# Optimization experiments

Hardware: AMD Instinct MI355X
Metric: run time of the kernel (lower is better)

## Reference

```python
import jax, jax.numpy as jnp
import numpy as np

N_HEAD = 16
N_KV_HEADS = 4
N_REP = 4
HEAD_DIM = 128
N_EMBD = 2048
EPS = 1e-5
ROPE_BASE = 10000.0


def setup_inputs() -> dict:
    key = jax.random.key(0)
    ks = jax.random.split(key, 5)
    B, T, C = 2, 2048, N_EMBD
    s = 0.02
    return {
        "x": jax.random.normal(ks[0], (B, T, C), dtype=jnp.float32),
        "wq": jax.random.normal(ks[1], (C, N_HEAD * HEAD_DIM), dtype=jnp.float32) * s,
        "wk": jax.random.normal(ks[2], (C, N_KV_HEADS * HEAD_DIM), dtype=jnp.float32) * s,
        "wv": jax.random.normal(ks[3], (C, N_KV_HEADS * HEAD_DIM), dtype=jnp.float32) * s,
        "wc": jax.random.normal(ks[4], (C, C), dtype=jnp.float32) * s,
        "q_norm_w": jnp.ones((HEAD_DIM,), dtype=jnp.float32),
        "k_norm_w": jnp.ones((HEAD_DIM,), dtype=jnp.float32),
    }


def _rmsnorm(x, w):
    # norm in fp32, scale by weight (matches RMSNorm.forward)
    xf = x.astype(jnp.float32)
    rms = jax.lax.rsqrt(jnp.mean(xf * xf, axis=-1, keepdims=True) + EPS)
    return (xf * rms).astype(x.dtype) * w


def _rope(x, cos, sin):
    # x: [B,T,H,D]; cos/sin: [T, D//2]; interleaved even/odd rotation
    xf = x.astype(jnp.float32)
    xe = xf[..., 0::2]
    xo = xf[..., 1::2]
    c = cos[None, :, None, :]
    s = sin[None, :, None, :]
    ye = xe * c - xo * s
    yo = xe * s + xo * c
    y = jnp.stack((ye, yo), axis=-1).reshape(x.shape)
    return y.astype(x.dtype)


def reference(x, wq, wk, wv, wc, q_norm_w, k_norm_w):
    B, T, C = x.shape
    q = (x @ wq).reshape(B, T, N_HEAD, HEAD_DIM)
    k = (x @ wk).reshape(B, T, N_KV_HEADS, HEAD_DIM)
    v = (x @ wv).reshape(B, T, N_KV_HEADS, HEAD_DIM)

    q = _rmsnorm(q, q_norm_w)
    k = _rmsnorm(k, k_norm_w)

    inv_freq = 1.0 / (ROPE_BASE ** (jnp.arange(0, HEAD_DIM, 2, dtype=jnp.float32) / HEAD_DIM))
    theta = jnp.arange(T, dtype=jnp.float32)[:, None] * inv_freq[None, :]  # [T, D//2]
    cos, sin = jnp.cos(theta), jnp.sin(theta)
    q = _rope(q, cos, sin)
    k = _rope(k, cos, sin)

    # GQA: repeat kv heads (repeat_kv with n_rep)
    k = jnp.repeat(k, N_REP, axis=2)  # [B,T,H,D]
    v = jnp.repeat(v, N_REP, axis=2)

    scale = 1.0 / jnp.sqrt(jnp.float32(HEAD_DIM))
    scores = jnp.einsum("bthd,bshd->bhts", q, k) * scale  # [B,H,T,S]
    causal = jnp.tril(jnp.ones((T, T), dtype=bool))
    scores = jnp.where(causal[None, None], scores, jnp.finfo(scores.dtype).min)
    attn = jax.nn.softmax(scores, axis=-1)
    y = jnp.einsum("bhts,bshd->bthd", attn, v).reshape(B, T, C)
    return y @ wc
```

## Files before the change

kernel.cpp:

```cpp
#include <hip/hip_runtime.h>
#include <hip/hip_bf16.h>
#include <cstdint>
#include <cstddef>

using bf16 = __hip_bfloat16;
typedef __attribute__((ext_vector_type(8))) short short8;
typedef __attribute__((ext_vector_type(4))) float f32x4;
typedef __attribute__((ext_vector_type(16))) float f32x16;

#define T_SEQ 2048
#define NHEAD 16
#define NKV 4
#define HD 128
#define CE 2048

__device__ __forceinline__ void gl_lds16(const void* g, void* l) {
  __builtin_amdgcn_global_load_lds(
      (const __attribute__((address_space(1))) unsigned int*)g,
      (__attribute__((address_space(3))) unsigned int*)l, 16, 0, 0);
}

__device__ __forceinline__ unsigned int cvtpk_bf16(float lo, float hi) {
  unsigned int r;
  asm("v_cvt_pk_bf16_f32 %0, %1, %2" : "=v"(r) : "v"(lo), "v"(hi));
  return r;
}

__device__ __forceinline__ void plswap(unsigned int& x, unsigned int& y, int hi) {
#if __has_builtin(__builtin_amdgcn_permlane32_swap)
  auto r = __builtin_amdgcn_permlane32_swap(x, y, false, false);
  x = r[0];
  y = r[1];
#else
  unsigned int xp = (unsigned int)__shfl_xor((int)x, 32);
  unsigned int yp = (unsigned int)__shfl_xor((int)y, 32);
  unsigned int nx = hi ? yp : x;
  unsigned int ny = hi ? y : xp;
  x = nx;
  y = ny;
#endif
}

__global__ void __launch_bounds__(256) cvt_bf16(const float* __restrict__ in,
                                                bf16* __restrict__ out, int n4) {
  const int i = blockIdx.x * blockDim.x + threadIdx.x;
  if (i >= n4) return;
  const float4 v = ((const float4*)in)[i];
  bf16 b0 = __float2bfloat16(v.x), b1 = __float2bfloat16(v.y),
       b2 = __float2bfloat16(v.z), b3 = __float2bfloat16(v.w);
  ushort4 u;
  u.x = *(const unsigned short*)&b0; u.y = *(const unsigned short*)&b1;
  u.z = *(const unsigned short*)&b2; u.w = *(const unsigned short*)&b3;
  ((ushort4*)out)[i] = u;
}

__global__ void __launch_bounds__(256) transpose_cvt(const float* __restrict__ W,
                                                     bf16* __restrict__ Wt, int N) {
  __shared__ float tile[32][33];
  const int tx = threadIdx.x & 31, ty = threadIdx.x >> 5;
  const int bx = blockIdx.x, by = blockIdx.y;
#pragma unroll
  for (int i = 0; i < 4; i++) {
    const int r = by * 32 + ty + i * 8;
    tile[ty + i * 8][tx] = W[(size_t)r * N + bx * 32 + tx];
  }
  __syncthreads();
#pragma unroll
  for (int i = 0; i < 4; i++) {
    const int n = bx * 32 + ty + i * 8;
    Wt[(size_t)n * 2048 + by * 32 + tx] = __float2bfloat16(tile[tx][ty + i * 8]);
  }
}

template <int BM, int BN, int WM, int WN>
__global__ void __launch_bounds__(512, 2)
gemm2p(const bf16* __restrict__ A, const bf16* __restrict__ Bt,
       float* __restrict__ C, int M, int N, int K) {
  constexpr int MF = BM / WM / 16;
  constexpr int NF = BN / WN / 16;
  constexpr int MH = MF / 2, NH = NF / 2;
  constexpr int AL = BM / 64;
  constexpr int BL = BN / 64;
  __shared__ bf16 smA[2][BM * 64];
  __shared__ bf16 smB[2][BN * 64];

  const int tid = threadIdx.x, lane = tid & 63, wid = tid >> 6;
  const int l15 = lane & 15, l4 = lane >> 4;
  const int wr = wid / WN, wc = wid % WN;

  const int nwg = gridDim.x;
  const int q = nwg >> 3, r = nwg & 7;
  const int xcd = blockIdx.x & 7, lin = blockIdx.x >> 3;
  const int wg = (xcd < r ? xcd * (q + 1) : r * (q + 1) + (xcd - r) * q) + lin;
  const int gw = N / BN;
  const int by = wg / gw, bx = wg % gw;
  const int row0 = by * BM, col0 = bx * BN;
  const int NT = K >> 6;

  const bf16* Ag = A + (size_t)row0 * K;
  const bf16* Bg = Bt + (size_t)col0 * K;

  auto stageA = [&](int t, int pbuf) {
    const int k0 = t << 6;
#pragma unroll
    for (int j = 0; j < AL; j++) {
      const int c = j * 512 + tid;
      const int rowi = c >> 3;
      gl_lds16(Ag + (size_t)rowi * K + k0 + (((c & 7) ^ (rowi & 7)) << 3),
               (void*)(&smA[pbuf][c << 3]));
    }
  };
  auto stageB = [&](int t, int pbuf) {
    const int k0 = t << 6;
#pragma unroll
    for (int j = 0; j < BL; j++) {
      const int c = j * 512 + tid;
      const int rowi = c >> 3;
      gl_lds16(Bg + (size_t)rowi * K + k0 + (((c & 7) ^ (rowi & 7)) << 3),
               (void*)(&smB[pbuf][c << 3]));
    }
  };

  f32x4 acc[MF][NF];
#pragma unroll
  for (int i = 0; i < MF; i++)
#pragma unroll
    for (int j = 0; j < NF; j++) acc[i][j] = (f32x4){0.f, 0.f, 0.f, 0.f};

  short8 a0[MH][2], a1[MH][2], bR[NF][2];

  stageA(0, 0);
  stageB(0, 0);
  stageA(1, 1);
  asm volatile("s_waitcnt vmcnt(%0)" ::"i"(AL) : "memory");
  __builtin_amdgcn_s_barrier();

  for (int t = 0; t < NT; ++t) {
    const int buf = t & 1;
    const bf16* sA = smA[buf];
    const bf16* sB = smB[buf];
    const int tB = (t + 1 < NT) ? t + 1 : NT - 1;
    const int tA = (t + 2 < NT) ? t + 2 : NT - 1;

    stageB(tB, buf ^ 1);

#pragma unroll
    for (int i = 0; i < MH; i++)
#pragma unroll
      for (int kk = 0; kk < 2; kk++) {
        const int lrow = wr * (BM / WM) + i * 16 + l15;
        a0[i][kk] = *(const short8*)(sA + lrow * 64 +
                                     ((((kk << 2) | l4) ^ (lrow & 7)) << 3));
      }
#pragma unroll
    for (int j = 0; j < NF; j++)
#pragma unroll
      for (int kk = 0; kk < 2; kk++) {
        const int lrow = wc * (BN / WN) + j * 16 + l15;
        bR[j][kk] = *(const short8*)(sB + lrow * 64 +
                                     ((((kk << 2) | l4) ^ (lrow & 7)) << 3));
      }

    __builtin_amdgcn_s_setprio(1);
#pragma unroll
    for (int i = 0; i < MH; i++)
#pragma unroll
      for (int j = 0; j < NH; j++)
#pragma unroll
        for (int kk = 0; kk < 2; kk++)
          acc[i][j] = __builtin_amdgcn_mfma_f32_16x16x32_bf16(
              a0[i][kk], bR[j][kk], acc[i][j], 0, 0, 0);
    __builtin_amdgcn_s_setprio(0);

#pragma unroll
    for (int i = 0; i < MH; i++)
#pragma unroll
      for (int kk = 0; kk < 2; kk++) {
        const int lrow = wr * (BM / WM) + (MH + i) * 16 + l15;
        a1[i][kk] = *(const short8*)(sA + lrow * 64 +
                                     ((((kk << 2) | l4) ^ (lrow & 7)) << 3));
      }

    __builtin_amdgcn_s_setprio(1);
#pragma unroll
    for (int i = 0; i < MH; i++)
#pragma unroll
      for (int j = 0; j < NH; j++)
#pragma unroll
        for (int kk = 0; kk < 2; kk++)
          acc[i][NH + j] = __builtin_amdgcn_mfma_f32_16x16x32_bf16(
              a0[i][kk], bR[NH + j][kk], acc[i][NH + j], 0, 0, 0);
#pragma unroll
    for (int i = 0; i < MH; i++)
#pragma unroll
      for (int j = 0; j < NH; j++)
#pragma unroll
        for (int kk = 0; kk < 2; kk++)
          acc[MH + i][NH + j] = __builtin_amdgcn_mfma_f32_16x16x32_bf16(
              a1[i][kk], bR[NH + j][kk], acc[MH + i][NH + j], 0, 0, 0);
    __builtin_amdgcn_s_setprio(0);

    __builtin_amdgcn_s_barrier();
    stageA(tA, buf);

    __builtin_amdgcn_s_setprio(1);
#pragma unroll
    for (int i = 0; i < MH; i++)
#pragma unroll
      for (int j = 0; j < NH; j++)
#pragma unroll
        for (int kk = 0; kk < 2; kk++)
          acc[MH + i][j] = __builtin_amdgcn_mfma_f32_16x16x32_bf16(
              a1[i][kk], bR[j][kk], acc[MH + i][j], 0, 0, 0);
    __builtin_amdgcn_s_setprio(0);

    asm volatile("s_waitcnt vmcnt(%0)" ::"i"(AL) : "memory");
    __builtin_amdgcn_s_barrier();
  }

#pragma unroll
  for (int i = 0; i < MF; i++)
#pragma unroll
    for (int j = 0; j < NF; j++)
#pragma unroll
      for (int rr = 0; rr < 4; rr++)
        C[(size_t)(row0 + wr * (BM / WM) + i * 16 + l4 * 4 + rr) * N +
          (col0 + wc * (BN / WN) + j * 16 + l15)] = acc[i][j][rr];

  asm volatile("s_waitcnt vmcnt(0)" ::: "memory");
}

__global__ void __launch_bounds__(256) qkv_post(const float* __restrict__ QKV,
                                                const float* __restrict__ qw,
                                                const float* __restrict__ kw,
                                                bf16* __restrict__ Qo,
                                                bf16* __restrict__ Ko,
                                                bf16* __restrict__ Vto) {
  const int g = blockIdx.x * 4 + (threadIdx.x >> 6);
  const int lane = threadIdx.x & 63;
  const int hh = g % 24;
  const int bt = g / 24;
  const int b = bt >> 11, t = bt & (T_SEQ - 1);
  int off;
  if (hh < 16) off = hh * 128;
  else if (hh < 20) off = 2048 + (hh - 16) * 128;
  else off = 2560 + (hh - 20) * 128;
  const float2 x = *(const float2*)(QKV + (size_t)bt * 3072 + off + lane * 2);
  if (hh < 20) {
    float ss = x.x * x.x + x.y * x.y;
    ss += __shfl_xor(ss, 1);  ss += __shfl_xor(ss, 2);  ss += __shfl_xor(ss, 4);
    ss += __shfl_xor(ss, 8);  ss += __shfl_xor(ss, 16); ss += __shfl_xor(ss, 32);
    const float rms = rsqrtf(ss * (1.0f / 128.0f) + 1e-5f);
    const float* w = (hh < 16) ? qw : kw;
    const float x0 = x.x * rms * w[lane * 2];
    const float x1 = x.y * rms * w[lane * 2 + 1];
    const float inv = exp2f((float)lane * (-13.287712379549449f / 64.0f));
    const float th = (float)t * inv;
    const float sn = sinf(th), cs = cosf(th);
    const float y0 = x0 * cs - x1 * sn;
    const float y1 = x0 * sn + x1 * cs;
    const bf16 o0 = __float2bfloat16(y0), o1 = __float2bfloat16(y1);
    if (hh < 16) {
      bf16* d = Qo + ((size_t)(b * NHEAD + hh) * T_SEQ + t) * HD + lane * 2;
      d[0] = o0; d[1] = o1;
    } else {
      bf16* d = Ko + ((size_t)(b * NKV + (hh - 16)) * T_SEQ + t) * HD + lane * 2;
      d[0] = o0; d[1] = o1;
    }
  } else {
    bf16* d = Vto + ((size_t)(b * NKV + (hh - 20)) * HD + lane * 2) * T_SEQ + t;
    d[0] = __float2bfloat16(x.x);
    d[T_SEQ] = __float2bfloat16(x.y);
  }
}

__global__ void __launch_bounds__(256, 2) attn_fwd(const bf16* __restrict__ Q,
                                                   const bf16* __restrict__ K,
                                                   const bf16* __restrict__ Vt,
                                                   bf16* __restrict__ Y) {
  __shared__ bf16 smK[128 * 128];
  __shared__ bf16 smV[128 * 128];

  const int bid = blockIdx.x;
  const int p = bid & 255, sdx = bid >> 8;
  const int bh = p & 31;
  const int jh = p >> 5;
  const int jq = sdx ? (15 - jh) : jh;
  const int h = bh & (NHEAD - 1), b = bh >> 4;
  const int bkv = b * NKV + (h >> 2);

  const int tid = threadIdx.x, wid = tid >> 6, lane = tid & 63;
  const int l31 = lane & 31, hi = lane >> 5;
  const int q0w = jq * 128 + wid * 32;

  const bf16* Kb = K + (size_t)bkv * T_SEQ * HD;
  const bf16* Vb = Vt + (size_t)bkv * HD * T_SEQ;

  const bf16* Qrow = Q + ((size_t)bh * T_SEQ + q0w + l31) * HD + hi * 8;
  short8 qf[8];
#pragma unroll
  for (int ds = 0; ds < 8; ds++) qf[ds] = *(const short8*)(Qrow + ds * 16);

  f32x16 o[4];
#pragma unroll
  for (int d = 0; d < 4; d++) o[d] = (f32x16)(0.f);
  float mrun = -INFINITY, lrun = 0.f;

  constexpr float CL = 0.08838834764831845f * 1.44269504088896340736f;
  const int trow = tid >> 4, tslot = tid & 15;

  for (int t = 0; t <= jq; t++) {
    const int k0 = t * 128;
    __syncthreads();
#pragma unroll
    for (int i = 0; i < 8; i++) {
      const int row = i * 16 + trow;
      const int ss = (tslot ^ (row & 15)) * 8;
      gl_lds16(Kb + (size_t)(k0 + row) * HD + ss, (void*)((char*)smK + i * 4096 + wid * 1024));
      gl_lds16(Vb + (size_t)row * T_SEQ + k0 + ss, (void*)((char*)smV + i * 4096 + wid * 1024));
    }
    __syncthreads();

    const bool lastt = (t == jq);
    const int glim = lastt ? wid : 3;

    f32x16 sg[4];
#pragma unroll
    for (int g = 0; g < 4; g++) {
      if (g > glim) continue;
      f32x16 acc = (f32x16)(0.f);
#pragma unroll
      for (int ds = 0; ds < 8; ds++) {
        const int row = g * 32 + l31;
        const short8 kf = *(const short8*)(smK + (size_t)row * 128 +
                                           (((ds << 1) | hi) ^ (row & 15)) * 8);
        acc = __builtin_amdgcn_mfma_f32_32x32x16_bf16(kf, qf[ds], acc, 0, 0, 0);
      }
      sg[g] = acc;
    }
    float tmax = -INFINITY;
#pragma unroll
    for (int g = 0; g < 4; g++) {
      if (g > glim) continue;
      if (lastt && g == wid) {
#pragma unroll
        for (int r = 0; r < 16; r++) {
          const int kr = (r & 3) + 8 * (r >> 2) + (hi << 2);
          if (kr > l31) sg[g][r] = -INFINITY;
        }
      }
#pragma unroll
      for (int r = 0; r < 16; r++) tmax = fmaxf(tmax, sg[g][r]);
    }
    tmax = fmaxf(tmax, __shfl_xor(tmax, 32));
    const float mnew = fmaxf(mrun, tmax);
    const float f = exp2f((mrun - mnew) * CL);
    mrun = mnew;
    lrun *= f;
#pragma unroll
    for (int d = 0; d < 4; d++)
#pragma unroll
      for (int r = 0; r < 16; r++) o[d][r] *= f;

    float lsum = 0.f;
#pragma unroll
    for (int g = 0; g < 4; g++) {
      if (g > glim) continue;
      float pp[16];
      float s0 = 0.f, s1 = 0.f;
#pragma unroll
      for (int r = 0; r < 16; r++) pp[r] = exp2f((sg[g][r] - mnew) * CL);
#pragma unroll
      for (int r = 0; r < 8; r++) { s0 += pp[2 * r]; s1 += pp[2 * r + 1]; }
      lsum += s0 + s1;

      unsigned int w0 = cvtpk_bf16(pp[0], pp[1]),  w2 = cvtpk_bf16(pp[4], pp[5]);
      unsigned int w1 = cvtpk_bf16(pp[2], pp[3]),  w3 = cvtpk_bf16(pp[6], pp[7]);
      unsigned int w4 = cvtpk_bf16(pp[8], pp[9]),  w6 = cvtpk_bf16(pp[12], pp[13]);
      unsigned int w5 = cvtpk_bf16(pp[10], pp[11]), w7 = cvtpk_bf16(pp[14], pp[15]);
      plswap(w0, w2, hi); plswap(w1, w3, hi);
      plswap(w4, w6, hi); plswap(w5, w7, hi);
      union { unsigned int u[4]; short8 s8; } pa0, pa1;
      pa0.u[0] = w0; pa0.u[1] = w1; pa0.u[2] = w2; pa0.u[3] = w3;
      pa1.u[0] = w4; pa1.u[1] = w5; pa1.u[2] = w6; pa1.u[3] = w7;

#pragma unroll
      for (int d = 0; d < 4; d++) {
        const int row = d * 32 + l31;
        const int ks0 = g * 2, ks1 = g * 2 + 1;
        const short8 vf0 = *(const short8*)(smV + (size_t)row * 128 +
                                            (((ks0 << 1) | hi) ^ (row & 15)) * 8);
        const short8 vf1 = *(const short8*)(smV + (size_t)row * 128 +
                                            (((ks1 << 1) | hi) ^ (row & 15)) * 8);
        o[d] = __builtin_amdgcn_mfma_f32_32x32x16_bf16(vf0, pa0.s8, o[d], 0, 0, 0);
        o[d] = __builtin_amdgcn_mfma_f32_32x32x16_bf16(vf1, pa1.s8, o[d], 0, 0, 0);
      }
    }
    lrun += lsum + __shfl_xor(lsum, 32);
  }

  const float inv = 1.0f / lrun;
  bf16* yrow = Y + ((size_t)(b * T_SEQ + q0w + l31)) * CE + h * HD;
#pragma unroll
  for (int d = 0; d < 4; d++) {
#pragma unroll
    for (int rg = 0; rg < 4; rg++) {
      ushort4 u;
      bf16 e0 = __float2bfloat16(o[d][rg * 4 + 0] * inv);
      bf16 e1 = __float2bfloat16(o[d][rg * 4 + 1] * inv);
      bf16 e2 = __float2bfloat16(o[d][rg * 4 + 2] * inv);
      bf16 e3 = __float2bfloat16(o[d][rg * 4 + 3] * inv);
      u.x = *(const unsigned short*)&e0; u.y = *(const unsigned short*)&e1;
      u.z = *(const unsigned short*)&e2; u.w = *(const unsigned short*)&e3;
      *(ushort4*)(yrow + d * 32 + rg * 8 + (hi << 2)) = u;
    }
  }
}

extern "C" void kernel_launch(void* const* d_in, const int* in_sizes, int n_in,
                              void* d_out, int out_size, void* d_ws, size_t ws_size,
                              hipStream_t stream) {
  const float* x   = (const float*)d_in[0];
  const float* wq  = (const float*)d_in[1];
  const float* wk  = (const float*)d_in[2];
  const float* wv  = (const float*)d_in[3];
  const float* wc  = (const float*)d_in[4];
  const float* qnw = (const float*)d_in[5];
  const float* knw = (const float*)d_in[6];
  float* out = (float*)d_out;

  char* ws = (char*)d_ws;
  bf16*  xb    = (bf16*)(ws);
  bf16*  wqkvt = (bf16*)(ws + 16777216);
  bf16*  wct   = (bf16*)(ws + 29360128);
  float* qkv   = (float*)(ws + 37748736);
  bf16*  Qb    = (bf16*)(ws + 88080384);
  bf16*  Kb    = (bf16*)(ws + 104857600);
  bf16*  Vtb   = (bf16*)(ws + 109051904);
  bf16*  yb    = (bf16*)(ws + 113246208);

  cvt_bf16<<<8192, 256, 0, stream>>>(x, xb, 2097152);
  transpose_cvt<<<dim3(64, 64), 256, 0, stream>>>(wq, wqkvt, 2048);
  transpose_cvt<<<dim3(16, 64), 256, 0, stream>>>(wk, wqkvt + (size_t)2048 * 2048, 512);
  transpose_cvt<<<dim3(16, 64), 256, 0, stream>>>(wv, wqkvt + (size_t)2560 * 2048, 512);
  transpose_cvt<<<dim3(64, 64), 256, 0, stream>>>(wc, wct, 2048);
  gemm2p<128, 256, 2, 4><<<384, 512, 0, stream>>>(xb, wqkvt, qkv, 4096, 3072, 2048);
  qkv_post<<<24576, 256, 0, stream>>>(qkv, qnw, knw, Qb, Kb, Vtb);
  attn_fwd<<<512, 256, 0, stream>>>(Qb, Kb, Vtb, yb);
  gemm2p<128, 256, 2, 4><<<256, 512, 0, stream>>>(yb, wct, out, 4096, 2048, 2048);
}
```

Measured before the change: 250.4 us.

## Restructure GEMM into four-quadrant pipelined loop and emit bf16 QKV output

Replaces the two-phase GEMM main loop with a four-quadrant schedule. Each tile is split into halves of A and B that are staged into LDS in smaller groups, and each quadrant's MFMAs are interleaved with barriers and partial vmcnt waits. The QKV projection now uses a 256x256 tile with 192 blocks and writes bf16 instead of fp32, which halves the intermediate write and the read in qkv_post. This trades extra barriers and lower grid occupancy for better load/compute overlap and less memory traffic, and rounds the QKV values to bf16 before RMSNorm.

```diff
diff --git a/kernel.cpp b/kernel.cpp
--- a/kernel.cpp
+++ b/kernel.cpp
@@ -72,15 +72,20 @@
   }
 }
 
-template <int BM, int BN, int WM, int WN>
+template <int BM, int BN, int WM, int WN, bool OBF>
 __global__ void __launch_bounds__(512, 2)
-gemm2p(const bf16* __restrict__ A, const bf16* __restrict__ Bt,
-       float* __restrict__ C, int M, int N, int K) {
-  constexpr int MF = BM / WM / 16;
-  constexpr int NF = BN / WN / 16;
-  constexpr int MH = MF / 2, NH = NF / 2;
+gemm4p(const bf16* __restrict__ A, const bf16* __restrict__ Bt,
+       void* __restrict__ Cv, int M, int N, int K) {
+  constexpr int AWS = BM / 2 / WM;
+  constexpr int BWS = BN / 2 / WN;
+  constexpr int MH = AWS / 16;
+  constexpr int NH = BWS / 16;
   constexpr int AL = BM / 64;
   constexpr int BL = BN / 64;
+  constexpr int AH = AL / 2;
+  constexpr int BH = BL / 2;
+  constexpr int G1N = AH + (BH + AH);
+  constexpr int G2N = BH;
   __shared__ bf16 smA[2][BM * 64];
   __shared__ bf16 smB[2][BN * 64];
 
@@ -100,137 +105,133 @@
   const bf16* Ag = A + (size_t)row0 * K;
   const bf16* Bg = Bt + (size_t)col0 * K;
 
-  auto stageA = [&](int t, int pbuf) {
+  auto stA = [&](int t, int h, int pb) {
     const int k0 = t << 6;
 #pragma unroll
-    for (int j = 0; j < AL; j++) {
-      const int c = j * 512 + tid;
+    for (int j = 0; j < AH; j++) {
+      const int c = (h * AH + j) * 512 + tid;
       const int rowi = c >> 3;
       gl_lds16(Ag + (size_t)rowi * K + k0 + (((c & 7) ^ (rowi & 7)) << 3),
-               (void*)(&smA[pbuf][c << 3]));
+               (void*)(&smA[pb][(size_t)c << 3]));
     }
   };
-  auto stageB = [&](int t, int pbuf) {
+  auto stB = [&](int t, int h, int pb) {
     const int k0 = t << 6;
 #pragma unroll
-    for (int j = 0; j < BL; j++) {
-      const int c = j * 512 + tid;
+    for (int j = 0; j < BH; j++) {
+      const int c = (h * BH + j) * 512 + tid;
       const int rowi = c >> 3;
       gl_lds16(Bg + (size_t)rowi * K + k0 + (((c & 7) ^ (rowi & 7)) << 3),
-               (void*)(&smB[pbuf][c << 3]));
+               (void*)(&smB[pb][(size_t)c << 3]));
     }
   };
-
-  f32x4 acc[MF][NF];
-#pragma unroll
-  for (int i = 0; i < MF; i++)
-#pragma unroll
-    for (int j = 0; j < NF; j++) acc[i][j] = (f32x4){0.f, 0.f, 0.f, 0.f};
-
-  short8 a0[MH][2], a1[MH][2], bR[NF][2];
-
-  stageA(0, 0);
-  stageB(0, 0);
-  stageA(1, 1);
-  asm volatile("s_waitcnt vmcnt(%0)" ::"i"(AL) : "memory");
+  auto rdA = [&](const bf16* sA, int mh, short8 (&dst)[MH][2]) {
+#pragma unroll
+    for (int i = 0; i < MH; i++) {
+      const int rowl = mh * (BM / 2) + wr * AWS + i * 16 + l15;
+#pragma unroll
+      for (int kk = 0; kk < 2; kk++)
+        dst[i][kk] = *(const short8*)(sA + rowl * 64 +
+                                      ((((kk << 2) | l4) ^ (rowl & 7)) << 3));
+    }
+  };
+  auto rdB = [&](const bf16* sB, int nh, short8 (&dst)[NH][2]) {
+#pragma unroll
+    for (int j = 0; j < NH; j++) {
+      const int rowl = nh * (BN / 2) + wc * BWS + j * 16 + l15;
+#pragma unroll
+      for (int kk = 0; kk < 2; kk++)
+        dst[j][kk] = *(const short8*)(sB + rowl * 64 +
+                                      ((((kk << 2) | l4) ^ (rowl & 7)) << 3));
+    }
+  };
+
+  f32x4 acc[2][2][MH][NH];
+#pragma unroll
+  for (int mh = 0; mh < 2; mh++)
+#pragma unroll
+    for (int nh = 0; nh < 2; nh++)
+#pragma unroll
+      for (int i = 0; i < MH; i++)
+#pragma unroll
+        for (int j = 0; j < NH; j++) acc[mh][nh][i][j] = (f32x4){0.f, 0.f, 0.f, 0.f};
+
+  auto mmq = [&](short8 (&a)[MH][2], short8 (&b)[NH][2], f32x4 (&ac)[MH][NH]) {
+    __builtin_amdgcn_s_setprio(1);
+#pragma unroll
+    for (int i = 0; i < MH; i++)
+#pragma unroll
+      for (int j = 0; j < NH; j++)
+#pragma unroll
+        for (int kk = 0; kk < 2; kk++)
+          ac[i][j] = __builtin_amdgcn_mfma_f32_16x16x32_bf16(a[i][kk], b[j][kk],
+                                                             ac[i][j], 0, 0, 0);
+    __builtin_amdgcn_s_setprio(0);
+  };
+
+  short8 a0[MH][2], a1[MH][2], b0[NH][2], b1[NH][2];
+
+  stA(0, 0, 0); stA(0, 1, 0); stB(0, 0, 0); stB(0, 1, 0);
+  asm volatile("s_waitcnt vmcnt(0)" ::: "memory");
   __builtin_amdgcn_s_barrier();
 
   for (int t = 0; t < NT; ++t) {
     const int buf = t & 1;
     const bf16* sA = smA[buf];
     const bf16* sB = smB[buf];
-    const int tB = (t + 1 < NT) ? t + 1 : NT - 1;
-    const int tA = (t + 2 < NT) ? t + 2 : NT - 1;
-
-    stageB(tB, buf ^ 1);
-
-#pragma unroll
-    for (int i = 0; i < MH; i++)
-#pragma unroll
-      for (int kk = 0; kk < 2; kk++) {
-        const int lrow = wr * (BM / WM) + i * 16 + l15;
-        a0[i][kk] = *(const short8*)(sA + lrow * 64 +
-                                     ((((kk << 2) | l4) ^ (lrow & 7)) << 3));
-      }
-#pragma unroll
-    for (int j = 0; j < NF; j++)
-#pragma unroll
-      for (int kk = 0; kk < 2; kk++) {
-        const int lrow = wc * (BN / WN) + j * 16 + l15;
-        bR[j][kk] = *(const short8*)(sB + lrow * 64 +
-                                     ((((kk << 2) | l4) ^ (lrow & 7)) << 3));
-      }
-
-    __builtin_amdgcn_s_setprio(1);
-#pragma unroll
-    for (int i = 0; i < MH; i++)
-#pragma unroll
-      for (int j = 0; j < NH; j++)
-#pragma unroll
-        for (int kk = 0; kk < 2; kk++)
-          acc[i][j] = __builtin_amdgcn_mfma_f32_16x16x32_bf16(
-              a0[i][kk], bR[j][kk], acc[i][j], 0, 0, 0);
-    __builtin_amdgcn_s_setprio(0);
-
-#pragma unroll
-    for (int i = 0; i < MH; i++)
-#pragma unroll
-      for (int kk = 0; kk < 2; kk++) {
-        const int lrow = wr * (BM / WM) + (MH + i) * 16 + l15;
-        a1[i][kk] = *(const short8*)(sA + lrow * 64 +
-                                     ((((kk << 2) | l4) ^ (lrow & 7)) << 3));
-      }
-
-    __builtin_amdgcn_s_setprio(1);
-#pragma unroll
-    for (int i = 0; i < MH; i++)
-#pragma unroll
-      for (int j = 0; j < NH; j++)
-#pragma unroll
-        for (int kk = 0; kk < 2; kk++)
-          acc[i][NH + j] = __builtin_amdgcn_mfma_f32_16x16x32_bf16(
-              a0[i][kk], bR[NH + j][kk], acc[i][NH + j], 0, 0, 0);
-#pragma unroll
-    for (int i = 0; i < MH; i++)
-#pragma unroll
-      for (int j = 0; j < NH; j++)
-#pragma unroll
-        for (int kk = 0; kk < 2; kk++)
-          acc[MH + i][NH + j] = __builtin_amdgcn_mfma_f32_16x16x32_bf16(
-              a1[i][kk], bR[NH + j][kk], acc[MH + i][NH + j], 0, 0, 0);
-    __builtin_amdgcn_s_setprio(0);
-
-    __builtin_amdgcn_s_barrier();
-    stageA(tA, buf);
-
-    __builtin_amdgcn_s_setprio(1);
-#pragma unroll
-    for (int i = 0; i < MH; i++)
-#pragma unroll
-      for (int j = 0; j < NH; j++)
-#pragma unroll
-        for (int kk = 0; kk < 2; kk++)
-          acc[MH + i][j] = __builtin_amdgcn_mfma_f32_16x16x32_bf16(
-              a1[i][kk], bR[j][kk], acc[MH + i][j], 0, 0, 0);
-    __builtin_amdgcn_s_setprio(0);
-
-    asm volatile("s_waitcnt vmcnt(%0)" ::"i"(AL) : "memory");
-    __builtin_amdgcn_s_barrier();
-  }
-
-#pragma unroll
-  for (int i = 0; i < MF; i++)
-#pragma unroll
-    for (int j = 0; j < NF; j++)
-#pragma unroll
-      for (int rr = 0; rr < 4; rr++)
-        C[(size_t)(row0 + wr * (BM / WM) + i * 16 + l4 * 4 + rr) * N +
-          (col0 + wc * (BN / WN) + j * 16 + l15)] = acc[i][j][rr];
+    const int tn = (t + 1 < NT) ? t + 1 : t;
+
+    stA(tn, 0, buf ^ 1);
+    rdA(sA, 0, a0);
+    rdB(sB, 0, b0);
+    __builtin_amdgcn_s_barrier();
+    asm volatile("s_waitcnt lgkmcnt(0)" ::: "memory");
+    __builtin_amdgcn_sched_barrier(0);
+    mmq(a0, b0, acc[0][0]);
+    __builtin_amdgcn_s_barrier();
+    stB(tn, 0, buf ^ 1);
+    stA(tn, 1, buf ^ 1);
+    rdA(sA, 1, a1);
+    __builtin_amdgcn_s_barrier();
+    asm volatile("s_waitcnt lgkmcnt(0)" ::: "memory");
+    __builtin_amdgcn_sched_barrier(0);
+    mmq(a1, b0, acc[1][0]);
+    asm volatile("s_waitcnt vmcnt(%0)" ::"i"(G1N) : "memory");
+    __builtin_amdgcn_s_barrier();
+    stB(tn, 1, buf ^ 1);
+    rdB(sB, 1, b1);
+    __builtin_amdgcn_s_barrier();
+    asm volatile("s_waitcnt lgkmcnt(0)" ::: "memory");
+    __builtin_amdgcn_sched_barrier(0);
+    mmq(a1, b1, acc[1][1]);
+    __builtin_amdgcn_s_barrier();
+    mmq(a0, b1, acc[0][1]);
+    asm volatile("s_waitcnt vmcnt(%0)" ::"i"(G2N) : "memory");
+    __builtin_amdgcn_s_barrier();
+  }
+
+#pragma unroll
+  for (int mh = 0; mh < 2; mh++)
+#pragma unroll
+    for (int nh = 0; nh < 2; nh++)
+#pragma unroll
+      for (int i = 0; i < MH; i++)
+#pragma unroll
+        for (int j = 0; j < NH; j++)
+#pragma unroll
+          for (int rr = 0; rr < 4; rr++) {
+            const size_t row = row0 + mh * (BM / 2) + wr * AWS + i * 16 + l4 * 4 + rr;
+            const size_t col = col0 + nh * (BN / 2) + wc * BWS + j * 16 + l15;
+            if constexpr (OBF)
+              ((bf16*)Cv)[row * N + col] = __float2bfloat16(acc[mh][nh][i][j][rr]);
+            else
+              ((float*)Cv)[row * N + col] = acc[mh][nh][i][j][rr];
+          }
 
   asm volatile("s_waitcnt vmcnt(0)" ::: "memory");
 }
 
-__global__ void __launch_bounds__(256) qkv_post(const float* __restrict__ QKV,
+__global__ void __launch_bounds__(256) qkv_post(const bf16* __restrict__ QKV,
                                                 const float* __restrict__ qw,
                                                 const float* __restrict__ kw,
                                                 bf16* __restrict__ Qo,
@@ -245,15 +246,17 @@
   if (hh < 16) off = hh * 128;
   else if (hh < 20) off = 2048 + (hh - 16) * 128;
   else off = 2560 + (hh - 20) * 128;
-  const float2 x = *(const float2*)(QKV + (size_t)bt * 3072 + off + lane * 2);
+  const ushort2 xr = *(const ushort2*)(QKV + (size_t)bt * 3072 + off + lane * 2);
+  const float xx = __bfloat162float(*(const bf16*)&xr.x);
+  const float xy = __bfloat162float(*(const bf16*)&xr.y);
   if (hh < 20) {
-    float ss = x.x * x.x + x.y * x.y;
+    float ss = xx * xx + xy * xy;
     ss += __shfl_xor(ss, 1);  ss += __shfl_xor(ss, 2);  ss += __shfl_xor(ss, 4);
     ss += __shfl_xor(ss, 8);  ss += __shfl_xor(ss, 16); ss += __shfl_xor(ss, 32);
     const float rms = rsqrtf(ss * (1.0f / 128.0f) + 1e-5f);
     const float* w = (hh < 16) ? qw : kw;
-    const float x0 = x.x * rms * w[lane * 2];
-    const float x1 = x.y * rms * w[lane * 2 + 1];
+    const float x0 = xx * rms * w[lane * 2];
+    const float x1 = xy * rms * w[lane * 2 + 1];
     const float inv = exp2f((float)lane * (-13.287712379549449f / 64.0f));
     const float th = (float)t * inv;
     const float sn = sinf(th), cs = cosf(th);
@@ -269,8 +272,8 @@
     }
   } else {
     bf16* d = Vto + ((size_t)(b * NKV + (hh - 20)) * HD + lane * 2) * T_SEQ + t;
-    d[0] = __float2bfloat16(x.x);
-    d[T_SEQ] = __float2bfloat16(x.y);
+    d[0] = __float2bfloat16(xx);
+    d[T_SEQ] = __float2bfloat16(xy);
   }
 }
 
@@ -433,7 +436,7 @@
   bf16*  xb    = (bf16*)(ws);
   bf16*  wqkvt = (bf16*)(ws + 16777216);
   bf16*  wct   = (bf16*)(ws + 29360128);
-  float* qkv   = (float*)(ws + 37748736);
+  bf16*  qkv   = (bf16*)(ws + 37748736);
   bf16*  Qb    = (bf16*)(ws + 88080384);
   bf16*  Kb    = (bf16*)(ws + 104857600);
   bf16*  Vtb   = (bf16*)(ws + 109051904);
@@ -444,8 +447,8 @@
   transpose_cvt<<<dim3(16, 64), 256, 0, stream>>>(wk, wqkvt + (size_t)2048 * 2048, 512);
   transpose_cvt<<<dim3(16, 64), 256, 0, stream>>>(wv, wqkvt + (size_t)2560 * 2048, 512);
   transpose_cvt<<<dim3(64, 64), 256, 0, stream>>>(wc, wct, 2048);
-  gemm2p<128, 256, 2, 4><<<384, 512, 0, stream>>>(xb, wqkvt, qkv, 4096, 3072, 2048);
+  gemm4p<256, 256, 2, 4, true><<<192, 512, 0, stream>>>(xb, wqkvt, qkv, 4096, 3072, 2048);
   qkv_post<<<24576, 256, 0, stream>>>(qkv, qnw, knw, Qb, Kb, Vtb);
   attn_fwd<<<512, 256, 0, stream>>>(Qb, Kb, Vtb, yb);
-  gemm2p<128, 256, 2, 4><<<256, 512, 0, stream>>>(yb, wct, out, 4096, 2048, 2048);
-}
+  gemm4p<128, 256, 2, 4, false><<<256, 512, 0, stream>>>(yb, wct, out, 4096, 2048, 2048);
+}
```

New measurement: 254.4 us. No clear change (+1.6%).
